# Optimization experiments

Measured on AMD Instinct MI355X. Metric: run time of the kernel, lower is better.

Reference implementation:

```python
import jax, jax.numpy as jnp
import numpy as np

I_T = 0.5       # IoU threshold self.I_t
GAMMA = 2.0     # focal loss gamma
EPS = 1e-7      # focal loss eps clamp
BS, P, C_IN = 8, 2048, 512


def pairwise_iou(b):
    # b: (bs, P, 4) xyxy -> (bs, P, P), same math as torchvision box_iou (no +1)
    area = (b[..., 2] - b[..., 0]) * (b[..., 3] - b[..., 1])
    lt = jnp.maximum(b[:, :, None, :2], b[:, None, :, :2])
    rb = jnp.minimum(b[:, :, None, 2:], b[:, None, :, 2:])
    wh = jnp.clip(rb - lt, 0.0, None)
    inter = wh[..., 0] * wh[..., 1]
    return inter / (area[:, :, None] + area[:, None, :] - inter)


def assign_labels_weights(pre_score, labels, rois):
    # Vectorized, order-faithful version of the per-batch/per-class python loop.
    # Selected seeds per class c: proposals with pre_score[...,c] > 0.5 if more than
    # one, else the single argmax proposal (torch code falls back when k<=1).
    # Sequential `_I > old` running max over (c, j) in ascending order is equivalent
    # to a global first-occurrence argmax (strict >), so per-class max + running
    # compare with earlier-class tie preference reproduces it exactly.
    bs, Pn = pre_score.shape[0], pre_score.shape[1]
    iou = pairwise_iou(rois)                      # (bs, P, P)
    run_I = jnp.full((bs, Pn), -1.0, pre_score.dtype)
    run_w = jnp.ones((bs, Pn), pre_score.dtype)
    hits = []
    for c in range(3):
        s = pre_score[:, :, c]                    # (bs, P)
        th = s > 0.5
        cnt = th.sum(-1)
        onehot = jnp.arange(Pn)[None, :] == jnp.argmax(s, -1)[:, None]
        sel = jnp.where((cnt > 1)[:, None], th, onehot)
        sel = sel & (labels[:, c] != 0)[:, None]  # skip classes absent from image
        masked = jnp.where(sel[:, None, :], iou, -2.0)  # (bs, P, P)
        val = masked.max(-1)                      # best IoU vs any seed of class c
        jidx = masked.argmax(-1)
        cand_x = jnp.take_along_axis(s, jidx, axis=1)
        better = val > run_I
        run_w = jnp.where(better, cand_x, run_w)
        run_I = jnp.where(better, val, run_I)
        hits.append(val > I_T)
    hit = jnp.stack(hits, -1)                     # (bs, P, 3)
    bg = (~hit.any(-1))[..., None]
    y = jnp.concatenate([hit.astype(pre_score.dtype), bg.astype(pre_score.dtype)], -1)
    return y, run_w


def icr_forward(inputs, fc_w, fc_b, pre_score, labels, rois, num):
    bs = inputs.shape[0] // num
    xr = inputs @ fc_w + fc_b                     # (bs*P, 4)
    logit = jax.nn.softmax(xr.reshape(bs, num, 4), -1)
    ps = jax.lax.stop_gradient(pre_score)         # .clone().detach()
    lb = jax.lax.stop_gradient(labels)
    y, w = assign_labels_weights(ps, lb, rois)
    y = y.reshape(bs * num, 4)
    w = w.reshape(bs * num, 1)
    # FocalLoss(gamma=2, mode='none')
    p = jnp.clip(jax.nn.softmax(xr, -1), EPS, 1.0 - EPS)
    fl = -y * jnp.log(p) * (1.0 - p) ** GAMMA
    imbalance = y.sum(0)                          # (4,)
    loss = (w * fl / (imbalance + 1e-7)).reshape(bs, num, 4)
    lab = lb.at[:, 3].set(1.0)[:, None, :]        # lab[:,0,3]=1
    w_ = 10.0 * jnp.exp(logit) * (1.0 - lab) + lab
    loss = (loss * w_).sum() / bs
    return logit, loss


def setup_inputs():
    key = jax.random.key(0)
    k = jax.random.split(key, 6)
    inputs = jax.random.normal(k[0], (BS * P, C_IN), jnp.float32)
    fc_w = jax.random.normal(k[1], (C_IN, 4), jnp.float32) * 0.02
    fc_b = jnp.zeros((4,), jnp.float32)
    pre_score = jax.random.uniform(k[2], (BS, P, 4), dtype=jnp.float32)
    labels = (jax.random.uniform(k[3], (BS, 4)) < 0.5).astype(jnp.float32)
    labels = labels.at[:, 3].set(0.0)
    xy = jax.random.uniform(k[4], (BS, P, 2), dtype=jnp.float32) * 448.0
    wh = jax.random.uniform(k[5], (BS, P, 2), dtype=jnp.float32) * 63.0 + 1.0
    rois = jnp.concatenate([xy, xy + wh], -1)     # valid xyxy boxes in 512x512
    return {"inputs": inputs, "fc_w": fc_w, "fc_b": fc_b, "pre_score": pre_score,
            "labels": labels, "rois": rois, "num": P}


def reference(inputs, fc_w, fc_b, pre_score, labels, rois, num):
    return icr_forward(inputs, fc_w, fc_b, pre_score, labels, rois, num)
```

## Files before the change

### kernel.cpp

```cpp
#include <hip/hip_runtime.h>

#define BSZ 8
#define PN  2048
#define CIN 512
#define CAP 2048
#define NW  16


__global__ __launch_bounds__(256) void k_front(
    const float* __restrict__ inp, const float* __restrict__ fcw,
    const float* __restrict__ fcb, const float* __restrict__ ps,
    const float* __restrict__ labels, const float* __restrict__ rois,
    float* __restrict__ logit, float* __restrict__ accum,
    int* __restrict__ meta, float* __restrict__ sList,
    float* __restrict__ areaL, float4* __restrict__ roiList)
{
  const int t = threadIdx.x;
  if (blockIdx.x < 1024) {
    const int gw   = (blockIdx.x * 256 + t) >> 6;
    const int lane = t & 63;
    const int kb   = lane << 2;
    const float4 wa0 = *(const float4*)(fcw + (kb + 0) * 4);
    const float4 wa1 = *(const float4*)(fcw + (kb + 1) * 4);
    const float4 wa2 = *(const float4*)(fcw + (kb + 2) * 4);
    const float4 wa3 = *(const float4*)(fcw + (kb + 3) * 4);
    const float4 wb0 = *(const float4*)(fcw + (256 + kb + 0) * 4);
    const float4 wb1 = *(const float4*)(fcw + (256 + kb + 1) * 4);
    const float4 wb2 = *(const float4*)(fcw + (256 + kb + 2) * 4);
    const float4 wb3 = *(const float4*)(fcw + (256 + kb + 3) * 4);
    const float4 bias = *(const float4*)fcb;
    #pragma unroll
    for (int rr = 0; rr < 4; ++rr) {
      const int r = (gw << 2) + rr;
      const float* row = inp + r * CIN;
      const float4 xa = *(const float4*)(row + kb);
      const float4 xb = *(const float4*)(row + 256 + kb);
      float a0 = xa.x*wa0.x + xa.y*wa1.x + xa.z*wa2.x + xa.w*wa3.x
               + xb.x*wb0.x + xb.y*wb1.x + xb.z*wb2.x + xb.w*wb3.x;
      float a1 = xa.x*wa0.y + xa.y*wa1.y + xa.z*wa2.y + xa.w*wa3.y
               + xb.x*wb0.y + xb.y*wb1.y + xb.z*wb2.y + xb.w*wb3.y;
      float a2 = xa.x*wa0.z + xa.y*wa1.z + xa.z*wa2.z + xa.w*wa3.z
               + xb.x*wb0.z + xb.y*wb1.z + xb.z*wb2.z + xb.w*wb3.z;
      float a3 = xa.x*wa0.w + xa.y*wa1.w + xa.z*wa2.w + xa.w*wa3.w
               + xb.x*wb0.w + xb.y*wb1.w + xb.z*wb2.w + xb.w*wb3.w;
      #pragma unroll
      for (int off = 32; off; off >>= 1) {
        a0 += __shfl_xor(a0, off); a1 += __shfl_xor(a1, off);
        a2 += __shfl_xor(a2, off); a3 += __shfl_xor(a3, off);
      }
      if (lane == 0) {
        a0 += bias.x; a1 += bias.y; a2 += bias.z; a3 += bias.w;
        const float m  = fmaxf(fmaxf(a0, a1), fmaxf(a2, a3));
        const float e0 = expf(a0 - m), e1 = expf(a1 - m);
        const float e2 = expf(a2 - m), e3 = expf(a3 - m);
        const float inv = 1.0f / (e0 + e1 + e2 + e3);
        float4 o; o.x = e0*inv; o.y = e1*inv; o.z = e2*inv; o.w = e3*inv;
        *(float4*)(logit + r * 4) = o;
      }
    }
    return;
  }

  const int bc = blockIdx.x - 1024;
  if (bc == 0 && t < 8) accum[t] = 0.0f;
  const int b = bc / 3;
  const int c = bc % 3;
  const int j0 = t * 8;

  float sv[8];
  int   flg = 0, cnt = 0;
  float vmax = -1e30f;
  int   jmax = 0;
  #pragma unroll
  for (int m = 0; m < 8; ++m) {
    const float s = ps[(b * PN + j0 + m) * 4 + c];
    sv[m] = s;
    if (s > 0.5f) { flg |= 1 << m; ++cnt; }
    if (s > vmax) { vmax = s; jmax = j0 + m; }
  }

  __shared__ float lv[256];
  __shared__ int   lj[256];
  __shared__ int   pre[256];
  lv[t] = vmax; lj[t] = jmax; pre[t] = cnt;
  __syncthreads();
  for (int off = 128; off > 0; off >>= 1) {
    if (t < off) {
      const float v2 = lv[t + off]; const int j2 = lj[t + off];
      if (v2 > lv[t] || (v2 == lv[t] && j2 < lj[t])) { lv[t] = v2; lj[t] = j2; }
    }
    __syncthreads();
  }
  for (int off = 1; off < 256; off <<= 1) {
    const int add = (t >= off) ? pre[t - off] : 0;
    __syncthreads();
    pre[t] += add;
    __syncthreads();
  }
  const int  totalTh = pre[255];
  const int  excl    = pre[t] - cnt;
  const int  jArg    = lj[0];
  const bool lab     = labels[b * 4 + c] != 0.0f;
  const int  L    = (!lab) ? 0 : ((totalTh > 1) ? totalTh : 1);
  const int  Lpad = (L + 7) & ~7;

  __shared__ float4 lastRoi;
  __shared__ float  lastS, lastA;
  float4* dstR = roiList + bc * CAP;
  float*  dstS = sList   + bc * CAP;
  float*  dstA = areaL   + bc * CAP;
  const float4* rb = ((const float4*)rois) + b * PN;

  if (lab) {
    if (totalTh > 1) {
      int pos = excl;
      #pragma unroll
      for (int m = 0; m < 8; ++m) {
        if (flg & (1 << m)) {
          const float4 r = rb[j0 + m];
          const float  a = (r.z - r.x) * (r.w - r.y);
          dstR[pos] = r; dstS[pos] = sv[m]; dstA[pos] = a;
          if (pos == L - 1) { lastRoi = r; lastS = sv[m]; lastA = a; }
          ++pos;
        }
      }
    } else if (t == (jArg >> 3)) {
      const float4 r = rb[jArg];
      const float  a = (r.z - r.x) * (r.w - r.y);
      dstR[0] = r; dstS[0] = sv[jArg & 7]; dstA[0] = a;
      lastRoi = r; lastS = sv[jArg & 7]; lastA = a;
    }
  }
  __syncthreads();
  if (t < Lpad - L) { dstR[L + t] = lastRoi; dstS[L + t] = lastS; dstA[L + t] = lastA; }
  if (t == 0) meta[bc] = Lpad;
}

__global__ __launch_bounds__(1024, 8) void k_assign(
    const float* __restrict__ rois, const int* __restrict__ meta,
    const float4* __restrict__ roiList, const float* __restrict__ areaL,
    float* __restrict__ pbn, float* __restrict__ pbd, int* __restrict__ pbp)
{
  const int blk   = blockIdx.x;
  const int h     = blk & 1;
  const int itile = (blk >> 1) & 31;
  const int b     = blk >> 6;
  const int t     = threadIdx.x;
  const int lane  = t & 63;
  const int wv    = t >> 6;

  __shared__ __align__(16) char ldsraw[61440];
  float4* sroi  = (float4*)ldsraw;
  float*  sarea = (float*)(ldsraw + 49152);
  float*  mn    = (float*)ldsraw;
  float*  md    = (float*)(ldsraw + 12288);
  int*    mp    = (int*)(ldsraw + 24576);

  int startc[3], cntc[3];
  #pragma unroll
  for (int c = 0; c < 3; ++c) {
    const int L  = meta[b * 3 + c];
    const int L2 = ((L >> 1) + 7) & ~7;
    const int s0 = h ? L2 : 0;
    const int e0 = h ? L  : L2;
    startc[c] = s0;
    cntc[c]   = e0 - s0;
    if (t < cntc[c]) {
      sroi [c * 1024 + t] = roiList[(b * 3 + c) * CAP + s0 + t];
      sarea[c * 1024 + t] = areaL  [(b * 3 + c) * CAP + s0 + t];
    }
  }
  const int i = (itile << 6) + lane;
  const float4 ri = ((const float4*)rois)[b * PN + i];
  const float areai = (ri.z - ri.x) * (ri.w - ri.y);
  __syncthreads();

  float BN[3], BD[3]; int BP[3];
  #pragma unroll
  for (int c = 0; c < 3; ++c) {
    const int cnt = cntc[c];
    const int C   = (((cnt + 15) >> 4) + 7) & ~7;
    const int g0  = wv * C;
    int g1 = g0 + C; if (g1 > cnt) g1 = cnt;
    float nA = -2.0f, dA = 1.0f, nB = -2.0f, dB = 1.0f;
    int   pA = 0, pB = 0;
    const float4* rbase = sroi  + c * 1024;
    const float*  abase = sarea + c * 1024;

    auto upd = [&](float& n, float& d, int& p,
                   const float4 rj, const float aj, const int pos) {
      const float lx = fmaxf(ri.x, rj.x), ly = fmaxf(ri.y, rj.y);
      const float rx = fminf(ri.z, rj.z), ry = fminf(ri.w, rj.w);
      const float ww = fmaxf(rx - lx, 0.0f), hh = fmaxf(ry - ly, 0.0f);
      const float inter = ww * hh;
      const float uni   = areai + aj - inter;
      if (inter * d > n * uni) { n = inter; d = uni; p = pos; }
    };

    for (int g = g0; g < g1; g += 4) {
      const float4 r0 = rbase[g], r1 = rbase[g+1], r2 = rbase[g+2], r3 = rbase[g+3];
      const float  a0 = abase[g], a1 = abase[g+1], a2 = abase[g+2], a3 = abase[g+3];
      upd(nA, dA, pA, r0, a0, g);
      upd(nB, dB, pB, r2, a2, g + 2);
      upd(nA, dA, pA, r1, a1, g + 1);
      upd(nB, dB, pB, r3, a3, g + 3);
    }
    const float tB = nB * dA, tA = nA * dB;
    if (tB > tA || (tB == tA && pB < pA)) { nA = nB; dA = dB; pA = pB; }
    BN[c] = nA; BD[c] = dA; BP[c] = pA + startc[c];
  }
  __syncthreads();
  #pragma unroll
  for (int c = 0; c < 3; ++c) {
    mn[(c * NW + wv) * 64 + lane] = BN[c];
    md[(c * NW + wv) * 64 + lane] = BD[c];
    mp[(c * NW + wv) * 64 + lane] = BP[c];
  }
  __syncthreads();
  if (wv == 0) {
    #pragma unroll
    for (int c = 0; c < 3; ++c) {
      float bn = BN[c], bd = BD[c]; int bp = BP[c];
      for (int w2 = 1; w2 < NW; ++w2) {
        const float n = mn[(c * NW + w2) * 64 + lane];
        const float d = md[(c * NW + w2) * 64 + lane];
        const int   p = mp[(c * NW + w2) * 64 + lane];
        if (n * bd > bn * d) { bn = n; bd = d; bp = p; }
      }
      const int o = ((b * 3 + c) * 2 + h) * PN + i;
      pbn[o] = bn; pbd[o] = bd; pbp[o] = bp;
    }
  }
}

__global__ __launch_bounds__(256) void k_back(
    const float* __restrict__ pbn, const float* __restrict__ pbd,
    const int* __restrict__ pbp, const float* __restrict__ sList,
    const float* __restrict__ logit, const float* __restrict__ labels,
    float* __restrict__ accum)
{
  const int t  = threadIdx.x;
  const int gi = blockIdx.x * 256 + t;
  const int b  = gi >> 11;
  const int i  = gi & (PN - 1);

  float v[3], sc[3];
  #pragma unroll
  for (int c = 0; c < 3; ++c) {
    const int o0 = ((b * 3 + c) * 2) * PN + i;
    float n = pbn[o0], d = pbd[o0]; int p = pbp[o0];
    const float n1 = pbn[o0 + PN], d1 = pbd[o0 + PN];
    const int   p1 = pbp[o0 + PN];
    if (n1 * d > n * d1) { n = n1; d = d1; p = p1; }
    v[c]  = n / d;
    sc[c] = sList[(b * 3 + c) * CAP + p];
  }
  float runI = -1.0f, runw = 1.0f;
  if (v[0] > runI) { runw = sc[0]; runI = v[0]; }
  if (v[1] > runI) { runw = sc[1]; runI = v[1]; }
  if (v[2] > runI) { runw = sc[2]; runI = v[2]; }
  const float y0 = (v[0] > 0.5f) ? 1.0f : 0.0f;
  const float y1 = (v[1] > 0.5f) ? 1.0f : 0.0f;
  const float y2 = (v[2] > 0.5f) ? 1.0f : 0.0f;
  const float y3 = (y0 + y1 + y2 == 0.0f) ? 1.0f : 0.0f;

  const float4 lg = ((const float4*)logit)[gi];
  const float lb0 = labels[b * 4 + 0];
  const float lb1 = labels[b * 4 + 1];
  const float lb2 = labels[b * 4 + 2];

  auto term = [&](const float l, const float yv, const float labv) -> float {
    const float p  = fminf(fmaxf(l, 1e-7f), 1.0f - 1e-7f);
    const float om = 1.0f - p;
    const float fl = -yv * logf(p) * om * om;
    const float wl = 10.0f * expf(l) * (1.0f - labv) + labv;
    return runw * fl * wl;
  };
  float s[8];
  s[0] = term(lg.x, y0, lb0); s[1] = term(lg.y, y1, lb1);
  s[2] = term(lg.z, y2, lb2); s[3] = term(lg.w, y3, 1.0f);
  s[4] = y0; s[5] = y1; s[6] = y2; s[7] = y3;

  #pragma unroll
  for (int k = 0; k < 8; ++k)
    #pragma unroll
    for (int off = 32; off; off >>= 1) s[k] += __shfl_xor(s[k], off);

  __shared__ float red[4][8];
  const int wv = t >> 6;
  if ((t & 63) == 0)
    #pragma unroll
    for (int k = 0; k < 8; ++k) red[wv][k] = s[k];
  __syncthreads();
  if (t < 8) {
    const float sum = red[0][t] + red[1][t] + red[2][t] + red[3][t];
    atomicAdd(&accum[t], sum);
  }
}

__global__ void k_final(const float* __restrict__ accum, float* __restrict__ loss)
{
  if (threadIdx.x == 0) {
    float L = 0.0f;
    #pragma unroll
    for (int c = 0; c < 4; ++c) L += accum[c] / (accum[4 + c] + 1e-7f);
    loss[0] = L * 0.125f;
  }
}

extern "C" void kernel_launch(void* const* d_in, const int* in_sizes, int n_in,
                              void* d_out, int out_size, void* d_ws, size_t ws_size,
                              hipStream_t stream)
{
  (void)in_sizes; (void)n_in; (void)out_size; (void)ws_size;
  const float* inp    = (const float*)d_in[0];
  const float* fcw    = (const float*)d_in[1];
  const float* fcb    = (const float*)d_in[2];
  const float* ps     = (const float*)d_in[3];
  const float* labels = (const float*)d_in[4];
  const float* rois   = (const float*)d_in[5];
  float* out = (float*)d_out;

  char* ws = (char*)d_ws;
  float*  accum   = (float*) (ws);
  int*    meta    = (int*)   (ws + 64);
  float*  sList   = (float*) (ws + 1024);
  float*  areaL   = (float*) (ws + 197632);
  float4* roiL    = (float4*)(ws + 394240);
  float*  pbn     = (float*) (ws + 1180672);
  float*  pbd     = (float*) (ws + 1573888);
  int*    pbp     = (int*)   (ws + 1967104);

  k_front <<<1048, 256, 0, stream>>>(inp, fcw, fcb, ps, labels, rois,
                                     out, accum, meta, sList, areaL, roiL);
  k_assign<<<512, 1024, 0, stream>>>(rois, meta, roiL, areaL, pbn, pbd, pbp);
  k_back  <<<64,   256, 0, stream>>>(pbn, pbd, pbp, sList, out, labels, accum);
  k_final <<<1,     64, 0, stream>>>(accum, out + BSZ * PN * 4);
}
```

Measured before the change: 117.6 us.

## Balance IoU assignment by splitting concatenated seed lists into equal chunks

The assignment kernel now concatenates all (batch, class) seed lists and splits the total into 64 equal chunks, each handled by 256-thread blocks over 32 row tiles. Before, each (batch, half) got fixed work, so load depended on how many seeds each class had. Partial results per (bc, chunk) are merged in the back kernel. The separate final kernel is folded into k_back through a last-block atomic counter, which saves one launch. The cost is a larger partial-result workspace, more scattered reads in the merge, and per-segment syncs inside each block.

New measurement: 123.8 us. 5.3% more time.

```diff
diff --git a/kernel.cpp b/kernel.cpp
--- a/kernel.cpp
+++ b/kernel.cpp
@@ -4,14 +4,15 @@
 #define PN  2048
 #define CIN 512
 #define CAP 2048
-#define NW  16
+#define NG  64
+#define KMAX 768
 
 
 __global__ __launch_bounds__(256) void k_front(
     const float* __restrict__ inp, const float* __restrict__ fcw,
     const float* __restrict__ fcb, const float* __restrict__ ps,
     const float* __restrict__ labels, const float* __restrict__ rois,
-    float* __restrict__ logit, float* __restrict__ accum,
+    float* __restrict__ logit, float* __restrict__ accum, int* __restrict__ cnt0,
     int* __restrict__ meta, float* __restrict__ sList,
     float* __restrict__ areaL, float4* __restrict__ roiList)
 {
@@ -62,7 +63,10 @@
   }
 
   const int bc = blockIdx.x - 1024;
-  if (bc == 0 && t < 8) accum[t] = 0.0f;
+  if (bc == 0) {
+    if (t < 8) accum[t] = 0.0f;
+    if (t == 8) *cnt0 = 0;
+  }
   const int b = bc / 3;
   const int c = bc % 3;
   const int j0 = t * 8;
@@ -136,124 +140,148 @@
   if (t == 0) meta[bc] = Lpad;
 }
 
-__global__ __launch_bounds__(1024, 8) void k_assign(
+__global__ __launch_bounds__(256, 8) void k_assign(
     const float* __restrict__ rois, const int* __restrict__ meta,
-    const float4* __restrict__ roiList, const float* __restrict__ areaL,
+    const float4* __restrict__ roiL, const float* __restrict__ areaL,
     float* __restrict__ pbn, float* __restrict__ pbd, int* __restrict__ pbp)
 {
-  const int blk   = blockIdx.x;
-  const int h     = blk & 1;
-  const int itile = (blk >> 1) & 31;
-  const int b     = blk >> 6;
+  const int g     = blockIdx.x >> 5;
+  const int itile = blockIdx.x & 31;
   const int t     = threadIdx.x;
   const int lane  = t & 63;
   const int wv    = t >> 6;
 
-  __shared__ __align__(16) char ldsraw[61440];
-  float4* sroi  = (float4*)ldsraw;
-  float*  sarea = (float*)(ldsraw + 49152);
-  float*  mn    = (float*)ldsraw;
-  float*  md    = (float*)(ldsraw + 12288);
-  int*    mp    = (int*)(ldsraw + 24576);
-
-  int startc[3], cntc[3];
-  #pragma unroll
-  for (int c = 0; c < 3; ++c) {
-    const int L  = meta[b * 3 + c];
-    const int L2 = ((L >> 1) + 7) & ~7;
-    const int s0 = h ? L2 : 0;
-    const int e0 = h ? L  : L2;
-    startc[c] = s0;
-    cntc[c]   = e0 - s0;
-    if (t < cntc[c]) {
-      sroi [c * 1024 + t] = roiList[(b * 3 + c) * CAP + s0 + t];
-      sarea[c * 1024 + t] = areaL  [(b * 3 + c) * CAP + s0 + t];
-    }
-  }
-  const int i = (itile << 6) + lane;
-  const float4 ri = ((const float4*)rois)[b * PN + i];
-  const float areai = (ri.z - ri.x) * (ri.w - ri.y);
-  __syncthreads();
-
-  float BN[3], BD[3]; int BP[3];
-  #pragma unroll
-  for (int c = 0; c < 3; ++c) {
-    const int cnt = cntc[c];
-    const int C   = (((cnt + 15) >> 4) + 7) & ~7;
-    const int g0  = wv * C;
-    int g1 = g0 + C; if (g1 > cnt) g1 = cnt;
+  int P[25];
+  P[0] = 0;
+  #pragma unroll
+  for (int k = 0; k < 24; ++k) P[k + 1] = P[k] + meta[k];
+  const int T = P[24];
+  const int K = (((T + NG - 1) / NG) + 7) & ~7;
+  const int s0 = g * K;
+  const int s1 = min(s0 + K, T);
+  if (s0 >= s1) return;
+
+  __shared__ float4 sroi[KMAX];
+  __shared__ float  sarea[KMAX];
+  __shared__ int    spos[KMAX];
+  __shared__ float  mrgN[4][64], mrgD[4][64];
+  __shared__ int    mrgP[4][64];
+
+  for (int idx = s0 + t; idx < s1; idx += 256) {
+    int bcs = 0;
+    while (idx >= P[bcs + 1]) ++bcs;
+    const int local = idx - P[bcs];
+    sroi [idx - s0] = roiL [bcs * CAP + local];
+    sarea[idx - s0] = areaL[bcs * CAP + local];
+    spos [idx - s0] = local;
+  }
+  __syncthreads();
+
+  auto upd = [](float& n, float& d, int& p, const float4 ri, const float areai,
+                const float4 rj, const float aj, const int pos) {
+    const float lx = fmaxf(ri.x, rj.x), ly = fmaxf(ri.y, rj.y);
+    const float rx = fminf(ri.z, rj.z), ry = fminf(ri.w, rj.w);
+    const float ww = fmaxf(rx - lx, 0.0f), hh = fmaxf(ry - ly, 0.0f);
+    const float inter = ww * hh;
+    const float uni   = areai + aj - inter;
+    if (inter * d > n * uni) { n = inter; d = uni; p = pos; }
+  };
+
+  int idx = s0;
+  int bc = 0;
+  while (idx >= P[bc + 1]) ++bc;
+  int curB = -1;
+  float4 ri = make_float4(0.f, 0.f, 0.f, 0.f);
+  float areai = 0.f;
+
+  while (idx < s1) {
+    const int e = min(s1, P[bc + 1]);
+    const int b = bc / 3;
+    if (b != curB) {
+      ri = ((const float4*)rois)[b * PN + (itile << 6) + lane];
+      areai = (ri.z - ri.x) * (ri.w - ri.y);
+      curB = b;
+    }
+    const int len = e - idx;
+    const int C   = ((len + 31) >> 5) << 3;
+    const int o0  = (idx - s0) + wv * C;
+    int o1 = o0 + C;
+    const int oe = e - s0;
+    if (o1 > oe) o1 = oe;
+
     float nA = -2.0f, dA = 1.0f, nB = -2.0f, dB = 1.0f;
     int   pA = 0, pB = 0;
-    const float4* rbase = sroi  + c * 1024;
-    const float*  abase = sarea + c * 1024;
-
-    auto upd = [&](float& n, float& d, int& p,
-                   const float4 rj, const float aj, const int pos) {
-      const float lx = fmaxf(ri.x, rj.x), ly = fmaxf(ri.y, rj.y);
-      const float rx = fminf(ri.z, rj.z), ry = fminf(ri.w, rj.w);
-      const float ww = fmaxf(rx - lx, 0.0f), hh = fmaxf(ry - ly, 0.0f);
-      const float inter = ww * hh;
-      const float uni   = areai + aj - inter;
-      if (inter * d > n * uni) { n = inter; d = uni; p = pos; }
-    };
-
-    for (int g = g0; g < g1; g += 4) {
-      const float4 r0 = rbase[g], r1 = rbase[g+1], r2 = rbase[g+2], r3 = rbase[g+3];
-      const float  a0 = abase[g], a1 = abase[g+1], a2 = abase[g+2], a3 = abase[g+3];
-      upd(nA, dA, pA, r0, a0, g);
-      upd(nB, dB, pB, r2, a2, g + 2);
-      upd(nA, dA, pA, r1, a1, g + 1);
-      upd(nB, dB, pB, r3, a3, g + 3);
-    }
-    const float tB = nB * dA, tA = nA * dB;
-    if (tB > tA || (tB == tA && pB < pA)) { nA = nB; dA = dB; pA = pB; }
-    BN[c] = nA; BD[c] = dA; BP[c] = pA + startc[c];
-  }
-  __syncthreads();
-  #pragma unroll
-  for (int c = 0; c < 3; ++c) {
-    mn[(c * NW + wv) * 64 + lane] = BN[c];
-    md[(c * NW + wv) * 64 + lane] = BD[c];
-    mp[(c * NW + wv) * 64 + lane] = BP[c];
-  }
-  __syncthreads();
-  if (wv == 0) {
-    #pragma unroll
-    for (int c = 0; c < 3; ++c) {
-      float bn = BN[c], bd = BD[c]; int bp = BP[c];
-      for (int w2 = 1; w2 < NW; ++w2) {
-        const float n = mn[(c * NW + w2) * 64 + lane];
-        const float d = md[(c * NW + w2) * 64 + lane];
-        const int   p = mp[(c * NW + w2) * 64 + lane];
-        if (n * bd > bn * d) { bn = n; bd = d; bp = p; }
-      }
-      const int o = ((b * 3 + c) * 2 + h) * PN + i;
-      pbn[o] = bn; pbd[o] = bd; pbp[o] = bp;
-    }
+    for (int o = o0; o < o1; o += 4) {
+      const float4 r0 = sroi[o],  r1 = sroi[o+1], r2 = sroi[o+2], r3 = sroi[o+3];
+      const float  a0 = sarea[o], a1 = sarea[o+1], a2 = sarea[o+2], a3 = sarea[o+3];
+      const int    q0 = spos[o],  q1 = spos[o+1],  q2 = spos[o+2],  q3 = spos[o+3];
+      upd(nA, dA, pA, ri, areai, r0, a0, q0);
+      upd(nB, dB, pB, ri, areai, r2, a2, q2);
+      upd(nA, dA, pA, ri, areai, r1, a1, q1);
+      upd(nB, dB, pB, ri, areai, r3, a3, q3);
+    }
+    { const float xB = nB * dA, xA = nA * dB;
+      if (xB > xA || (xB == xA && pB < pA)) { nA = nB; dA = dB; pA = pB; } }
+
+    __syncthreads();
+    mrgN[wv][lane] = nA; mrgD[wv][lane] = dA; mrgP[wv][lane] = pA;
+    __syncthreads();
+    if (wv == 0) {
+      float n = mrgN[0][lane], d = mrgD[0][lane]; int p = mrgP[0][lane];
+      #pragma unroll
+      for (int w = 1; w < 4; ++w) {
+        const float n2 = mrgN[w][lane], d2 = mrgD[w][lane];
+        const int   p2 = mrgP[w][lane];
+        const float x2 = n2 * d, x1 = n * d2;
+        if (x2 > x1 || (x2 == x1 && p2 < p)) { n = n2; d = d2; p = p2; }
+      }
+      const int o = (bc * NG + g) * PN + (itile << 6) + lane;
+      pbn[o] = n; pbd[o] = d; pbp[o] = p;
+    }
+    idx = e; ++bc;
   }
 }
 
 __global__ __launch_bounds__(256) void k_back(
     const float* __restrict__ pbn, const float* __restrict__ pbd,
-    const int* __restrict__ pbp, const float* __restrict__ sList,
-    const float* __restrict__ logit, const float* __restrict__ labels,
-    float* __restrict__ accum)
+    const int* __restrict__ pbp, const int* __restrict__ meta,
+    const float* __restrict__ sList, const float* __restrict__ logit,
+    const float* __restrict__ labels, float* __restrict__ accum,
+    int* __restrict__ cnt0, float* __restrict__ loss)
 {
   const int t  = threadIdx.x;
   const int gi = blockIdx.x * 256 + t;
   const int b  = gi >> 11;
   const int i  = gi & (PN - 1);
 
+  int P[25];
+  P[0] = 0;
+  #pragma unroll
+  for (int k = 0; k < 24; ++k) P[k + 1] = P[k] + meta[k];
+  const int T = P[24];
+  const int K = (((T + NG - 1) / NG) + 7) & ~7;
+
   float v[3], sc[3];
   #pragma unroll
   for (int c = 0; c < 3; ++c) {
-    const int o0 = ((b * 3 + c) * 2) * PN + i;
-    float n = pbn[o0], d = pbd[o0]; int p = pbp[o0];
-    const float n1 = pbn[o0 + PN], d1 = pbd[o0 + PN];
-    const int   p1 = pbp[o0 + PN];
-    if (n1 * d > n * d1) { n = n1; d = d1; p = p1; }
-    v[c]  = n / d;
-    sc[c] = sList[(b * 3 + c) * CAP + p];
+    const int bc = b * 3 + c;
+    const int Pb0 = P[bc], Pb1 = P[bc + 1];
+    float n = -2.0f, d = 1.0f; int p = 0;
+    if (Pb1 > Pb0) {
+      const int gs = Pb0 / K;
+      const int ge = (Pb1 + K - 1) / K;
+      for (int g = gs; g < ge; ++g) {
+        const int o = (bc * NG + g) * PN + i;
+        const float n2 = pbn[o], d2 = pbd[o];
+        const int   p2 = pbp[o];
+        const float x2 = n2 * d, x1 = n * d2;
+        if (x2 > x1 || (x2 == x1 && p2 < p)) { n = n2; d = d2; p = p2; }
+      }
+      v[c]  = n / d;
+      sc[c] = sList[bc * CAP + p];
+    } else {
+      v[c] = -2.0f; sc[c] = 1.0f;
+    }
   }
   float runI = -1.0f, runw = 1.0f;
   if (v[0] > runI) { runw = sc[0]; runI = v[0]; }
@@ -270,9 +298,9 @@
   const float lb2 = labels[b * 4 + 2];
 
   auto term = [&](const float l, const float yv, const float labv) -> float {
-    const float p  = fminf(fmaxf(l, 1e-7f), 1.0f - 1e-7f);
-    const float om = 1.0f - p;
-    const float fl = -yv * logf(p) * om * om;
+    const float p2 = fminf(fmaxf(l, 1e-7f), 1.0f - 1e-7f);
+    const float om = 1.0f - p2;
+    const float fl = -yv * logf(p2) * om * om;
     const float wl = 10.0f * expf(l) * (1.0f - labv) + labv;
     return runw * fl * wl;
   };
@@ -296,15 +324,18 @@
     const float sum = red[0][t] + red[1][t] + red[2][t] + red[3][t];
     atomicAdd(&accum[t], sum);
   }
-}
-
-__global__ void k_final(const float* __restrict__ accum, float* __restrict__ loss)
-{
-  if (threadIdx.x == 0) {
-    float L = 0.0f;
-    #pragma unroll
-    for (int c = 0; c < 4; ++c) L += accum[c] / (accum[4 + c] + 1e-7f);
-    loss[0] = L * 0.125f;
+  __syncthreads();
+  if (t == 0) {
+    __threadfence();
+    if (atomicAdd(cnt0, 1) == 63) {
+      float a[8];
+      #pragma unroll
+      for (int k = 0; k < 8; ++k) a[k] = atomicAdd(&accum[k], 0.0f);
+      float L = 0.0f;
+      #pragma unroll
+      for (int c = 0; c < 4; ++c) L += a[c] / (a[4 + c] + 1e-7f);
+      loss[0] = L * 0.125f;
+    }
   }
 }
 
@@ -322,18 +353,19 @@
   float* out = (float*)d_out;
 
   char* ws = (char*)d_ws;
-  float*  accum   = (float*) (ws);
-  int*    meta    = (int*)   (ws + 64);
-  float*  sList   = (float*) (ws + 1024);
-  float*  areaL   = (float*) (ws + 197632);
-  float4* roiL    = (float4*)(ws + 394240);
-  float*  pbn     = (float*) (ws + 1180672);
-  float*  pbd     = (float*) (ws + 1573888);
-  int*    pbp     = (int*)   (ws + 1967104);
+  float*  accum = (float*) (ws);
+  int*    cnt0  = (int*)   (ws + 32);
+  int*    meta  = (int*)   (ws + 64);
+  float*  sList = (float*) (ws + 1024);
+  float*  areaL = (float*) (ws + 197632);
+  float4* roiL  = (float4*)(ws + 394240);
+  float*  pbn   = (float*) (ws + 1180672);
+  float*  pbd   = (float*) (ws + 13763584);
+  int*    pbp   = (int*)   (ws + 26346496);
 
   k_front <<<1048, 256, 0, stream>>>(inp, fcw, fcb, ps, labels, rois,
-                                     out, accum, meta, sList, areaL, roiL);
-  k_assign<<<512, 1024, 0, stream>>>(rois, meta, roiL, areaL, pbn, pbd, pbp);
-  k_back  <<<64,   256, 0, stream>>>(pbn, pbd, pbp, sList, out, labels, accum);
-  k_final <<<1,     64, 0, stream>>>(accum, out + BSZ * PN * 4);
+                                     out, accum, cnt0, meta, sList, areaL, roiL);
+  k_assign<<<NG * 32, 256, 0, stream>>>(rois, meta, roiL, areaL, pbn, pbd, pbp);
+  k_back  <<<64, 256, 0, stream>>>(pbn, pbd, pbp, meta, sList, out, labels,
+                                   accum, cnt0, out + BSZ * PN * 4);
 }
```

## Stream seed boxes from global memory, recompute areas, fold final kernel into back

Applied to the files above, without the earlier changes.

The assign kernel stops staging the seed ROI list and areas in LDS. Each wave now reads the boxes straight from global memory (wave-uniform addresses, so effectively broadcast through cache) and recomputes each seed's area inline, with the loop unrolled to 8. The separate area list is dropped from the front kernel, and the one-block final kernel is merged into the back kernel using a last-block-done atomic counter. This cuts LDS use and one sync per block, a launch, and some memory traffic, at the cost of extra ALU work and global loads in the inner loop. It also adds an index tie-break when merging the two halves.

New measurement: 130.0 us. +10.6%, slower.

```diff
diff --git a/kernel.cpp b/kernel.cpp
--- a/kernel.cpp
+++ b/kernel.cpp
@@ -11,9 +11,9 @@
     const float* __restrict__ inp, const float* __restrict__ fcw,
     const float* __restrict__ fcb, const float* __restrict__ ps,
     const float* __restrict__ labels, const float* __restrict__ rois,
-    float* __restrict__ logit, float* __restrict__ accum,
+    float* __restrict__ logit, float* __restrict__ accum, int* __restrict__ cnt0,
     int* __restrict__ meta, float* __restrict__ sList,
-    float* __restrict__ areaL, float4* __restrict__ roiList)
+    float4* __restrict__ roiList)
 {
   const int t = threadIdx.x;
   if (blockIdx.x < 1024) {
@@ -62,7 +62,10 @@
   }
 
   const int bc = blockIdx.x - 1024;
-  if (bc == 0 && t < 8) accum[t] = 0.0f;
+  if (bc == 0) {
+    if (t < 8) accum[t] = 0.0f;
+    if (t == 8) *cnt0 = 0;
+  }
   const int b = bc / 3;
   const int c = bc % 3;
   const int j0 = t * 8;
@@ -105,10 +108,9 @@
   const int  Lpad = (L + 7) & ~7;
 
   __shared__ float4 lastRoi;
-  __shared__ float  lastS, lastA;
+  __shared__ float  lastS;
   float4* dstR = roiList + bc * CAP;
   float*  dstS = sList   + bc * CAP;
-  float*  dstA = areaL   + bc * CAP;
   const float4* rb = ((const float4*)rois) + b * PN;
 
   if (lab) {
@@ -118,27 +120,25 @@
       for (int m = 0; m < 8; ++m) {
         if (flg & (1 << m)) {
           const float4 r = rb[j0 + m];
-          const float  a = (r.z - r.x) * (r.w - r.y);
-          dstR[pos] = r; dstS[pos] = sv[m]; dstA[pos] = a;
-          if (pos == L - 1) { lastRoi = r; lastS = sv[m]; lastA = a; }
+          dstR[pos] = r; dstS[pos] = sv[m];
+          if (pos == L - 1) { lastRoi = r; lastS = sv[m]; }
           ++pos;
         }
       }
     } else if (t == (jArg >> 3)) {
       const float4 r = rb[jArg];
-      const float  a = (r.z - r.x) * (r.w - r.y);
-      dstR[0] = r; dstS[0] = sv[jArg & 7]; dstA[0] = a;
-      lastRoi = r; lastS = sv[jArg & 7]; lastA = a;
-    }
-  }
-  __syncthreads();
-  if (t < Lpad - L) { dstR[L + t] = lastRoi; dstS[L + t] = lastS; dstA[L + t] = lastA; }
+      dstR[0] = r; dstS[0] = sv[jArg & 7];
+      lastRoi = r; lastS = sv[jArg & 7];
+    }
+  }
+  __syncthreads();
+  if (t < Lpad - L) { dstR[L + t] = lastRoi; dstS[L + t] = lastS; }
   if (t == 0) meta[bc] = Lpad;
 }
 
 __global__ __launch_bounds__(1024, 8) void k_assign(
     const float* __restrict__ rois, const int* __restrict__ meta,
-    const float4* __restrict__ roiList, const float* __restrict__ areaL,
+    const float4* __restrict__ roiL,
     float* __restrict__ pbn, float* __restrict__ pbd, int* __restrict__ pbp)
 {
   const int blk   = blockIdx.x;
@@ -149,86 +149,73 @@
   const int lane  = t & 63;
   const int wv    = t >> 6;
 
-  __shared__ __align__(16) char ldsraw[61440];
-  float4* sroi  = (float4*)ldsraw;
-  float*  sarea = (float*)(ldsraw + 49152);
-  float*  mn    = (float*)ldsraw;
-  float*  md    = (float*)(ldsraw + 12288);
-  int*    mp    = (int*)(ldsraw + 24576);
-
-  int startc[3], cntc[3];
+  __shared__ float mn[3][NW][64];
+  __shared__ float md[3][NW][64];
+  __shared__ int   mp[3][NW][64];
+
+  const int i = (itile << 6) + lane;
+  const float4 ri = ((const float4*)rois)[b * PN + i];
+  const float areai = (ri.z - ri.x) * (ri.w - ri.y);
+
+  auto upd = [&](float& n, float& d, int& p,
+                 const float4 rj, const int pos) {
+    const float lx = fmaxf(ri.x, rj.x), ly = fmaxf(ri.y, rj.y);
+    const float rx = fminf(ri.z, rj.z), ry = fminf(ri.w, rj.w);
+    const float ww = fmaxf(rx - lx, 0.0f), hh = fmaxf(ry - ly, 0.0f);
+    const float inter = ww * hh;
+    const float aj    = (rj.z - rj.x) * (rj.w - rj.y);
+    const float uni   = areai + aj - inter;
+    if (inter * d > n * uni) { n = inter; d = uni; p = pos; }
+  };
+
+  float BN[3], BD[3]; int BP[3];
   #pragma unroll
   for (int c = 0; c < 3; ++c) {
     const int L  = meta[b * 3 + c];
     const int L2 = ((L >> 1) + 7) & ~7;
     const int s0 = h ? L2 : 0;
     const int e0 = h ? L  : L2;
-    startc[c] = s0;
-    cntc[c]   = e0 - s0;
-    if (t < cntc[c]) {
-      sroi [c * 1024 + t] = roiList[(b * 3 + c) * CAP + s0 + t];
-      sarea[c * 1024 + t] = areaL  [(b * 3 + c) * CAP + s0 + t];
-    }
-  }
-  const int i = (itile << 6) + lane;
-  const float4 ri = ((const float4*)rois)[b * PN + i];
-  const float areai = (ri.z - ri.x) * (ri.w - ri.y);
-  __syncthreads();
-
-  float BN[3], BD[3]; int BP[3];
-  #pragma unroll
-  for (int c = 0; c < 3; ++c) {
-    const int cnt = cntc[c];
+    const int cnt = e0 - s0;
     const int C   = (((cnt + 15) >> 4) + 7) & ~7;
     const int g0  = wv * C;
     int g1 = g0 + C; if (g1 > cnt) g1 = cnt;
+
     float nA = -2.0f, dA = 1.0f, nB = -2.0f, dB = 1.0f;
     int   pA = 0, pB = 0;
-    const float4* rbase = sroi  + c * 1024;
-    const float*  abase = sarea + c * 1024;
-
-    auto upd = [&](float& n, float& d, int& p,
-                   const float4 rj, const float aj, const int pos) {
-      const float lx = fmaxf(ri.x, rj.x), ly = fmaxf(ri.y, rj.y);
-      const float rx = fminf(ri.z, rj.z), ry = fminf(ri.w, rj.w);
-      const float ww = fmaxf(rx - lx, 0.0f), hh = fmaxf(ry - ly, 0.0f);
-      const float inter = ww * hh;
-      const float uni   = areai + aj - inter;
-      if (inter * d > n * uni) { n = inter; d = uni; p = pos; }
-    };
-
-    for (int g = g0; g < g1; g += 4) {
-      const float4 r0 = rbase[g], r1 = rbase[g+1], r2 = rbase[g+2], r3 = rbase[g+3];
-      const float  a0 = abase[g], a1 = abase[g+1], a2 = abase[g+2], a3 = abase[g+3];
-      upd(nA, dA, pA, r0, a0, g);
-      upd(nB, dB, pB, r2, a2, g + 2);
-      upd(nA, dA, pA, r1, a1, g + 1);
-      upd(nB, dB, pB, r3, a3, g + 3);
-    }
-    const float tB = nB * dA, tA = nA * dB;
-    if (tB > tA || (tB == tA && pB < pA)) { nA = nB; dA = dB; pA = pB; }
-    BN[c] = nA; BD[c] = dA; BP[c] = pA + startc[c];
-  }
-  __syncthreads();
+    const float4* base = roiL + (b * 3 + c) * CAP + s0;
+    for (int g = g0; g < g1; g += 8) {
+      float4 r[8];
+      #pragma unroll
+      for (int u = 0; u < 8; ++u) r[u] = base[g + u];
+      upd(nA, dA, pA, r[0], g + 0);
+      upd(nB, dB, pB, r[4], g + 4);
+      upd(nA, dA, pA, r[1], g + 1);
+      upd(nB, dB, pB, r[5], g + 5);
+      upd(nA, dA, pA, r[2], g + 2);
+      upd(nB, dB, pB, r[6], g + 6);
+      upd(nA, dA, pA, r[3], g + 3);
+      upd(nB, dB, pB, r[7], g + 7);
+    }
+    { const float xB = nB * dA, xA = nA * dB;
+      if (xB > xA || (xB == xA && pB < pA)) { nA = nB; dA = dB; pA = pB; } }
+    BN[c] = nA; BD[c] = dA; BP[c] = pA + s0;
+  }
   #pragma unroll
   for (int c = 0; c < 3; ++c) {
-    mn[(c * NW + wv) * 64 + lane] = BN[c];
-    md[(c * NW + wv) * 64 + lane] = BD[c];
-    mp[(c * NW + wv) * 64 + lane] = BP[c];
+    mn[c][wv][lane] = BN[c]; md[c][wv][lane] = BD[c]; mp[c][wv][lane] = BP[c];
   }
   __syncthreads();
   if (wv == 0) {
     #pragma unroll
     for (int c = 0; c < 3; ++c) {
-      float bn = BN[c], bd = BD[c]; int bp = BP[c];
+      float n = BN[c], d = BD[c]; int p = BP[c];
       for (int w2 = 1; w2 < NW; ++w2) {
-        const float n = mn[(c * NW + w2) * 64 + lane];
-        const float d = md[(c * NW + w2) * 64 + lane];
-        const int   p = mp[(c * NW + w2) * 64 + lane];
-        if (n * bd > bn * d) { bn = n; bd = d; bp = p; }
+        const float n2 = mn[c][w2][lane], d2 = md[c][w2][lane];
+        const int   p2 = mp[c][w2][lane];
+        if (n2 * d > n * d2) { n = n2; d = d2; p = p2; }
       }
       const int o = ((b * 3 + c) * 2 + h) * PN + i;
-      pbn[o] = bn; pbd[o] = bd; pbp[o] = bp;
+      pbn[o] = n; pbd[o] = d; pbp[o] = p;
     }
   }
 }
@@ -237,7 +224,8 @@
     const float* __restrict__ pbn, const float* __restrict__ pbd,
     const int* __restrict__ pbp, const float* __restrict__ sList,
     const float* __restrict__ logit, const float* __restrict__ labels,
-    float* __restrict__ accum)
+    float* __restrict__ accum, int* __restrict__ cnt0,
+    float* __restrict__ loss)
 {
   const int t  = threadIdx.x;
   const int gi = blockIdx.x * 256 + t;
@@ -247,13 +235,15 @@
   float v[3], sc[3];
   #pragma unroll
   for (int c = 0; c < 3; ++c) {
-    const int o0 = ((b * 3 + c) * 2) * PN + i;
+    const int bc = b * 3 + c;
+    const int o0 = (bc * 2) * PN + i;
     float n = pbn[o0], d = pbd[o0]; int p = pbp[o0];
     const float n1 = pbn[o0 + PN], d1 = pbd[o0 + PN];
     const int   p1 = pbp[o0 + PN];
-    if (n1 * d > n * d1) { n = n1; d = d1; p = p1; }
+    const float x1 = n1 * d, x0 = n * d1;
+    if (x1 > x0 || (x1 == x0 && p1 < p)) { n = n1; d = d1; p = p1; }
     v[c]  = n / d;
-    sc[c] = sList[(b * 3 + c) * CAP + p];
+    sc[c] = sList[bc * CAP + p];
   }
   float runI = -1.0f, runw = 1.0f;
   if (v[0] > runI) { runw = sc[0]; runI = v[0]; }
@@ -270,9 +260,9 @@
   const float lb2 = labels[b * 4 + 2];
 
   auto term = [&](const float l, const float yv, const float labv) -> float {
-    const float p  = fminf(fmaxf(l, 1e-7f), 1.0f - 1e-7f);
-    const float om = 1.0f - p;
-    const float fl = -yv * logf(p) * om * om;
+    const float p2 = fminf(fmaxf(l, 1e-7f), 1.0f - 1e-7f);
+    const float om = 1.0f - p2;
+    const float fl = -yv * logf(p2) * om * om;
     const float wl = 10.0f * expf(l) * (1.0f - labv) + labv;
     return runw * fl * wl;
   };
@@ -296,15 +286,18 @@
     const float sum = red[0][t] + red[1][t] + red[2][t] + red[3][t];
     atomicAdd(&accum[t], sum);
   }
-}
-
-__global__ void k_final(const float* __restrict__ accum, float* __restrict__ loss)
-{
-  if (threadIdx.x == 0) {
-    float L = 0.0f;
-    #pragma unroll
-    for (int c = 0; c < 4; ++c) L += accum[c] / (accum[4 + c] + 1e-7f);
-    loss[0] = L * 0.125f;
+  __syncthreads();
+  if (t == 0) {
+    __threadfence();
+    if (atomicAdd(cnt0, 1) == 63) {
+      float a[8];
+      #pragma unroll
+      for (int k = 0; k < 8; ++k) a[k] = atomicAdd(&accum[k], 0.0f);
+      float L = 0.0f;
+      #pragma unroll
+      for (int c = 0; c < 4; ++c) L += a[c] / (a[4 + c] + 1e-7f);
+      loss[0] = L * 0.125f;
+    }
   }
 }
 
@@ -322,18 +315,18 @@
   float* out = (float*)d_out;
 
   char* ws = (char*)d_ws;
-  float*  accum   = (float*) (ws);
-  int*    meta    = (int*)   (ws + 64);
-  float*  sList   = (float*) (ws + 1024);
-  float*  areaL   = (float*) (ws + 197632);
-  float4* roiL    = (float4*)(ws + 394240);
-  float*  pbn     = (float*) (ws + 1180672);
-  float*  pbd     = (float*) (ws + 1573888);
-  int*    pbp     = (int*)   (ws + 1967104);
+  float*  accum = (float*) (ws);
+  int*    cnt0  = (int*)   (ws + 32);
+  int*    meta  = (int*)   (ws + 64);
+  float*  sList = (float*) (ws + 1024);
+  float4* roiL  = (float4*)(ws + 197632);
+  float*  pbn   = (float*) (ws + 984064);
+  float*  pbd   = (float*) (ws + 1377280);
+  int*    pbp   = (int*)   (ws + 1770496);
 
   k_front <<<1048, 256, 0, stream>>>(inp, fcw, fcb, ps, labels, rois,
-                                     out, accum, meta, sList, areaL, roiL);
-  k_assign<<<512, 1024, 0, stream>>>(rois, meta, roiL, areaL, pbn, pbd, pbp);
-  k_back  <<<64,   256, 0, stream>>>(pbn, pbd, pbp, sList, out, labels, accum);
-  k_final <<<1,     64, 0, stream>>>(accum, out + BSZ * PN * 4);
+                                     out, accum, cnt0, meta, sList, roiL);
+  k_assign<<<512, 1024, 0, stream>>>(rois, meta, roiL, pbn, pbd, pbp);
+  k_back  <<<64,   256, 0, stream>>>(pbn, pbd, pbp, sList, out, labels,
+                                     accum, cnt0, out + BSZ * PN * 4);
 }
```
